# Kernel tuning notes

Measured on AMD Instinct MI355X. Metric: run time of the kernel, lower is better.

Reference implementation:

```python
import math
import jax, jax.numpy as jnp
import numpy as np

B, S, E = 4, 2048, 1024

def setup_inputs() -> dict:
    key = jax.random.key(0)
    k1, k2, k3 = jax.random.split(key, 3)
    X = jax.random.normal(k1, (B, S, E), dtype=jnp.float32)
    # nn.Linear(E, 3E): weight [3E, E], bias [3E]; scale weights for sane softmax
    W = jax.random.normal(k2, (3 * E, E), dtype=jnp.float32) * (1.0 / math.sqrt(E))
    b = jax.random.normal(k3, (3 * E,), dtype=jnp.float32) * 0.01
    return {"X": X, "W": W, "b": b}

def reference(X, W, b):
    E_ = X.shape[-1]
    # fused QKV projection: X @ W^T + b -> [B, S, 3E]
    qkv = jnp.einsum('bse,fe->bsf', X, W) + b
    q, k, v = jnp.split(qkv, 3, axis=-1)
    scores = jnp.einsum('bqe,bke->bqk', q, k) / math.sqrt(E_)
    attention_weight = jax.nn.softmax(scores, axis=-1)  # [B, S, S]
    output = jnp.einsum('bqk,bke->bqe', attention_weight, v)
    return (output, attention_weight)
```

## Files before the change

kernel.cpp:

```cpp
#include <hip/hip_runtime.h>
#include <math.h>

typedef __bf16 bf16;
typedef __bf16 bf16x4 __attribute__((ext_vector_type(4)));
typedef __bf16 bf16x8 __attribute__((ext_vector_type(8)));
typedef float f32x4 __attribute__((ext_vector_type(4)));

#define MODE_QKV    0
#define MODE_SCORES 1
#define MODE_PV     2

__device__ inline void gload_lds16(const bf16* g, bf16* l) {
    __builtin_amdgcn_global_load_lds(
        (const __attribute__((address_space(1))) void*)g,
        (__attribute__((address_space(3))) void*)l, 16, 0, 0);
}

#define DSR(dst, base, imm)                                                 \
    asm volatile("ds_read_b128 %0, %1 offset:%2"                            \
        : "=v"(dst)                                                         \
        : "v"((const __attribute__((address_space(3))) bf16*)(base)),       \
          "i"(imm))

#define MF(i, j) acc[i][j] = __builtin_amdgcn_mfma_f32_16x16x32_bf16(       \
    af[i], bq[j], acc[i][j], 0, 0, 0);

template <int MODE, int NT>
__global__ __launch_bounds__(512) void mfma_nt(
    const bf16* __restrict__ A, const bf16* __restrict__ B,
    const float* __restrict__ bias, void* __restrict__ Cv,
    int lda, int ldb, int ldc,
    long sA, long sB, long sC, float alpha)
{
    A += (long)blockIdx.z * sA;
    B += (long)blockIdx.z * sB;

    __shared__ bf16 As[3 * 8192] __attribute__((aligned(16)));
    __shared__ bf16 Bs[3 * 4096] __attribute__((aligned(16)));

    const int t  = threadIdx.x;
    const int m0 = blockIdx.y * 256;
    const int n0 = blockIdx.x * 128;

    const int lane = t & 63;
    const int wave = t >> 6;
    const int wr   = (wave >> 1) * 64;
    const int wc   = (wave & 1) * 64;
    const int fr   = lane & 15;
    const int kq8  = lane >> 4;

    const bf16* gA0; const bf16* gA1; const bf16* gB0;
    {
        const int c0 = t,        r0 = c0 >> 2, h0 = ((c0 & 3) ^ ((r0 >> 1) & 3)) * 8;
        const int c1 = t + 512,  r1 = c1 >> 2, h1 = ((c1 & 3) ^ ((r1 >> 1) & 3)) * 8;
        gA0 = A + (long)(m0 + r0) * lda + h0;
        gA1 = A + (long)(m0 + r1) * lda + h1;
        gB0 = B + (long)(n0 + r0) * ldb + h0;
    }

    const int swz = kq8 ^ ((fr >> 1) & 3);
    const bf16* pA = As + (wr + fr) * 32 + swz * 8;
    const bf16* pB = Bs + (wc + fr) * 32 + swz * 8;

    f32x4 acc[4][4] = {};
    bf16x8 af[4], bq[4];
    int kofs;

#define STAGE3(SS, ko)                                                      \
    gload_lds16(gA0 + (ko), &As[(SS) * 8192 + t * 8]);                      \
    gload_lds16(gA1 + (ko), &As[(SS) * 8192 + (t + 512) * 8]);              \
    gload_lds16(gB0 + (ko), &Bs[(SS) * 4096 + t * 8]);

#define TB(CS, STG) do {                                                    \
    DSR(af[0], pA, (CS) * 16384 + 0);                                       \
    DSR(af[1], pA, (CS) * 16384 + 1024);                                    \
    DSR(bq[0], pB, (CS) * 8192 + 0);                                        \
    DSR(bq[1], pB, (CS) * 8192 + 1024);                                     \
    DSR(bq[2], pB, (CS) * 8192 + 2048);                                     \
    DSR(bq[3], pB, (CS) * 8192 + 3072);                                     \
    DSR(af[2], pA, (CS) * 16384 + 2048);                                    \
    DSR(af[3], pA, (CS) * 16384 + 3072);                                    \
    asm volatile("s_waitcnt lgkmcnt(2)" ::: "memory");                      \
    __builtin_amdgcn_sched_barrier(0);                                      \
    __builtin_amdgcn_s_setprio(1);                                          \
    MF(0,0) MF(0,1) MF(1,0) MF(1,1)                                         \
    MF(0,2) MF(0,3) MF(1,2) MF(1,3)                                         \
    __builtin_amdgcn_s_setprio(0);                                          \
    if constexpr ((STG) == 1) { STAGE3(((CS) + 2) % 3, kofs); kofs += 32; } \
    asm volatile("s_waitcnt lgkmcnt(0)" ::: "memory");                      \
    __builtin_amdgcn_sched_barrier(0);                                      \
    __builtin_amdgcn_s_setprio(1);                                          \
    MF(2,0) MF(2,1) MF(3,0) MF(3,1)                                         \
    MF(2,2) MF(2,3) MF(3,2) MF(3,3)                                         \
    __builtin_amdgcn_s_setprio(0);                                          \
    if constexpr ((STG) == 1)                                               \
        asm volatile("s_waitcnt vmcnt(3)" ::: "memory");                    \
    else if constexpr ((STG) == 0)                                          \
        asm volatile("s_waitcnt vmcnt(0)" ::: "memory");                    \
    if constexpr ((STG) != 2) __builtin_amdgcn_s_barrier();                 \
} while (0)

    STAGE3(0, 0);
    STAGE3(1, 32);
    kofs = 64;
    asm volatile("s_waitcnt vmcnt(3)" ::: "memory");
    __builtin_amdgcn_s_barrier();

    static_assert(NT % 3 != 0, "peel pattern assumes NT%3 in {1,2}");
    if constexpr (NT % 3 == 2) {
        TB(0, 1); TB(1, 1);
        for (int g = 0; g < (NT - 5) / 3; ++g) { TB(2, 1); TB(0, 1); TB(1, 1); }
        TB(2, 1); TB(0, 0); TB(1, 2);
    } else {
        TB(0, 1);
        for (int g = 0; g < (NT - 4) / 3; ++g) { TB(1, 1); TB(2, 1); TB(0, 1); }
        TB(1, 1); TB(2, 0); TB(0, 2);
    }
#undef TB
#undef STAGE3

    const int r4 = (lane >> 4) * 4;
    if constexpr (MODE == MODE_PV) {
        float* C = (float*)Cv + (long)blockIdx.z * sC;
#pragma unroll
        for (int j = 0; j < 4; j++) {
            const int col = n0 + wc + j * 16 + fr;
#pragma unroll
            for (int i = 0; i < 4; i++)
#pragma unroll
                for (int r = 0; r < 4; r++) {
                    const long row = m0 + wr + i * 16 + r4 + r;
                    C[row * ldc + col] = acc[i][j][r];
                }
        }
    } else {
        bf16* C = (bf16*)Cv + (long)blockIdx.z * sC;
#pragma unroll
        for (int j = 0; j < 4; j++) {
            const int col = n0 + wc + j * 16 + fr;
            const float bv = (MODE == MODE_QKV) ? bias[col] : 0.f;
#pragma unroll
            for (int i = 0; i < 4; i++)
#pragma unroll
                for (int r = 0; r < 4; r++) {
                    const long row = m0 + wr + i * 16 + r4 + r;
                    float v = acc[i][j][r];
                    if constexpr (MODE == MODE_QKV)
                        C[row * ldc + col] = (bf16)(v + bv);
                    else
                        C[row * ldc + col] = (bf16)__expf(alpha * v);
                }
        }
    }
}

__global__ __launch_bounds__(256) void f32_to_bf16(
    const float* __restrict__ in, bf16* __restrict__ out, long n)
{
    long i = ((long)blockIdx.x * 256 + threadIdx.x) * 4;
    if (i < n) {
        float4 v = *(const float4*)(in + i);
        bf16x4 o = { (bf16)v.x, (bf16)v.y, (bf16)v.z, (bf16)v.w };
        *(bf16x4*)(out + i) = o;
    }
}

__global__ __launch_bounds__(256) void transpose_v(
    const bf16* __restrict__ V, bf16* __restrict__ Vt)
{
    __shared__ bf16 tile[32][33];
    const bf16* Vb  = V  + (long)blockIdx.z * 2048 * 3072;
    bf16*       Vtb = Vt + (long)blockIdx.z * 1024 * 2048;
    const int s0 = blockIdx.x * 32, e0 = blockIdx.y * 32;
    const int tx = threadIdx.x & 31, ty = threadIdx.x >> 5;
#pragma unroll
    for (int i = 0; i < 32; i += 8)
        tile[ty + i][tx] = Vb[(long)(s0 + ty + i) * 3072 + e0 + tx];
    __syncthreads();
#pragma unroll
    for (int i = 0; i < 32; i += 8)
        Vtb[(long)(e0 + ty + i) * 2048 + s0 + tx] = tile[tx][ty + i];
}

__global__ __launch_bounds__(256) void norm_rows(
    bf16* __restrict__ Pu, float* __restrict__ out1)
{
    bf16* p  = Pu   + (long)blockIdx.x * 2048;
    float* o = out1 + (long)blockIdx.x * 2048;
    const int t = threadIdx.x;
    bf16x8 v = *(const bf16x8*)(p + t * 8);
    float f[8];
    float s = 0.f;
#pragma unroll
    for (int k = 0; k < 8; k++) { f[k] = (float)v[k]; s += f[k]; }
#pragma unroll
    for (int off = 32; off > 0; off >>= 1) s += __shfl_xor(s, off);
    __shared__ float red[4];
    const int wid = t >> 6, lane = t & 63;
    if (lane == 0) red[wid] = s;
    __syncthreads();
    s = red[0] + red[1] + red[2] + red[3];
    const float inv = 1.0f / s;
    float4 a, b;
    a.x = f[0] * inv; a.y = f[1] * inv; a.z = f[2] * inv; a.w = f[3] * inv;
    b.x = f[4] * inv; b.y = f[5] * inv; b.z = f[6] * inv; b.w = f[7] * inv;
    *(float4*)(o + t * 8)     = a;
    *(float4*)(o + t * 8 + 4) = b;
    bf16x8 w;
#pragma unroll
    for (int k = 0; k < 8; k++) w[k] = (bf16)(f[k] * inv);
    *(bf16x8*)(p + t * 8) = w;
}

extern "C" void kernel_launch(void* const* d_in, const int* in_sizes, int n_in,
                              void* d_out, int out_size, void* d_ws, size_t ws_size,
                              hipStream_t stream)
{
    const int B = 4, S = 2048, E = 1024;
    const float* X    = (const float*)d_in[0];
    const float* W    = (const float*)d_in[1];
    const float* bias = (const float*)d_in[2];

    float* out0 = (float*)d_out;
    float* out1 = out0 + (long)B * S * E;

    char* ws = (char*)d_ws;
    bf16* qkvb = (bf16*)(ws);
    bf16* Vt   = (bf16*)(ws + 50331648);
    bf16* Pu   = (bf16*)(ws + 67108864);
    bf16* Xb   = (bf16*)(ws + 67108864);
    bf16* Wb   = (bf16*)(ws + 83886080);

    f32_to_bf16<<<(long)B * S * E / 1024, 256, 0, stream>>>(X, Xb, (long)B * S * E);
    f32_to_bf16<<<(long)3 * E * E / 1024, 256, 0, stream>>>(W, Wb, (long)3 * E * E);

    mfma_nt<MODE_QKV, 32><<<dim3(3 * E / 128, B * S / 256, 1), 512, 0, stream>>>(
        Xb, Wb, bias, qkvb, E, E, 3 * E, 0, 0, 0, 1.0f);

    transpose_v<<<dim3(S / 32, E / 32, B), 256, 0, stream>>>(qkvb + 2 * E, Vt);

    mfma_nt<MODE_SCORES, 32><<<dim3(S / 128, S / 256, B), 512, 0, stream>>>(
        qkvb, qkvb + E, nullptr, Pu, 3 * E, 3 * E, S,
        (long)S * 3 * E, (long)S * 3 * E, (long)S * S, 0.03125f);

    norm_rows<<<B * S, 256, 0, stream>>>(Pu, out1);

    mfma_nt<MODE_PV, 64><<<dim3(E / 128, S / 256, B), 512, 0, stream>>>(
        Pu, Vt, nullptr, out0, S, S, E,
        (long)S * S, (long)E * S, (long)S * E, 1.0f);
}
```

Baseline: 296.7 us.

## Add 256x256-tile GEMM kernel with 4-stage ring for QKV and scores

Adds a new mfma_nt256 kernel that computes 256x256 output tiles, with each wave owning 128x64. It uses a 4-deep LDS ring buffer and split A/B staging interleaved with two MFMA half-phases. The QKV projection and score GEMMs now launch this kernel with half as many blocks along N, which raises arithmetic intensity per LDS byte. The cost is double the accumulator registers (128 floats per thread), 128KB of LDS, extra barriers, and fewer blocks for occupancy and load balance.

```diff
diff --git a/kernel.cpp b/kernel.cpp
--- a/kernel.cpp
+++ b/kernel.cpp
@@ -24,6 +24,133 @@
 
 #define MF(i, j) acc[i][j] = __builtin_amdgcn_mfma_f32_16x16x32_bf16(       \
     af[i], bq[j], acc[i][j], 0, 0, 0);
+
+template <int MODE, int NT>
+__global__ __launch_bounds__(512) void mfma_nt256(
+    const bf16* __restrict__ A, const bf16* __restrict__ B,
+    const float* __restrict__ bias, void* __restrict__ Cv,
+    int lda, int ldb, int ldc,
+    long sA, long sB, long sC, float alpha)
+{
+    A += (long)blockIdx.z * sA;
+    B += (long)blockIdx.z * sB;
+
+    __shared__ bf16 As[4 * 8192] __attribute__((aligned(16)));
+    __shared__ bf16 Bs[4 * 8192] __attribute__((aligned(16)));
+
+    const int t  = threadIdx.x;
+    const int m0 = blockIdx.y * 256;
+    const int n0 = blockIdx.x * 256;
+
+    const int lane = t & 63;
+    const int wave = t >> 6;
+    const int wr   = (wave >> 2) * 128;
+    const int wc   = (wave & 3) * 64;
+    const int fr   = lane & 15;
+    const int kq8  = lane >> 4;
+
+    const bf16* gA0; const bf16* gA1; const bf16* gB0; const bf16* gB1;
+    {
+        const int c0 = t,        r0 = c0 >> 2, h0 = ((c0 & 3) ^ ((r0 >> 1) & 3)) * 8;
+        const int c1 = t + 512,  r1 = c1 >> 2, h1 = ((c1 & 3) ^ ((r1 >> 1) & 3)) * 8;
+        gA0 = A + (long)(m0 + r0) * lda + h0;
+        gA1 = A + (long)(m0 + r1) * lda + h1;
+        gB0 = B + (long)(n0 + r0) * ldb + h0;
+        gB1 = B + (long)(n0 + r1) * ldb + h1;
+    }
+
+    const int swz = kq8 ^ ((fr >> 1) & 3);
+    const bf16* pA = As + (wr + fr) * 32 + swz * 8;
+    const bf16* pB = Bs + (wc + fr) * 32 + swz * 8;
+
+    f32x4 acc[8][4] = {};
+    bf16x8 af[8], bq[4];
+    int kofs;
+
+#define STA256(SS, ko)                                                      \
+    gload_lds16(gA0 + (ko), &As[(SS) * 8192 + t * 8]);                      \
+    gload_lds16(gA1 + (ko), &As[(SS) * 8192 + (t + 512) * 8]);
+#define STB256(SS, ko)                                                      \
+    gload_lds16(gB0 + (ko), &Bs[(SS) * 8192 + t * 8]);                      \
+    gload_lds16(gB1 + (ko), &Bs[(SS) * 8192 + (t + 512) * 8]);
+
+#define TB256(S, STG) do {                                                  \
+               \
+    DSR(af[0], pA, (S) * 16384 + 0);                                        \
+    DSR(af[1], pA, (S) * 16384 + 1024);                                     \
+    DSR(af[2], pA, (S) * 16384 + 2048);                                     \
+    DSR(af[3], pA, (S) * 16384 + 3072);                                     \
+    DSR(bq[0], pB, (S) * 16384 + 0);                                        \
+    DSR(bq[1], pB, (S) * 16384 + 1024);                                     \
+    DSR(bq[2], pB, (S) * 16384 + 2048);                                     \
+    DSR(bq[3], pB, (S) * 16384 + 3072);                                     \
+    if constexpr ((STG) == 1) { STA256(((S) + 3) & 3, kofs); }              \
+    __builtin_amdgcn_s_barrier();                                           \
+    asm volatile("s_waitcnt lgkmcnt(0)" ::: "memory");                      \
+    __builtin_amdgcn_sched_barrier(0);                                      \
+    __builtin_amdgcn_s_setprio(1);                                          \
+    MF(0,0) MF(0,1) MF(0,2) MF(0,3) MF(1,0) MF(1,1) MF(1,2) MF(1,3)         \
+    MF(2,0) MF(2,1) MF(2,2) MF(2,3) MF(3,0) MF(3,1) MF(3,2) MF(3,3)         \
+    __builtin_amdgcn_s_setprio(0);                                          \
+    __builtin_amdgcn_s_barrier();                                           \
+                       \
+    DSR(af[4], pA, (S) * 16384 + 4096);                                     \
+    DSR(af[5], pA, (S) * 16384 + 5120);                                     \
+    DSR(af[6], pA, (S) * 16384 + 6144);                                     \
+    DSR(af[7], pA, (S) * 16384 + 7168);                                     \
+    if constexpr ((STG) == 1) { STB256(((S) + 3) & 3, kofs); kofs += 32; }  \
+    __builtin_amdgcn_s_barrier();                                           \
+    asm volatile("s_waitcnt lgkmcnt(0)" ::: "memory");                      \
+    __builtin_amdgcn_sched_barrier(0);                                      \
+    __builtin_amdgcn_s_setprio(1);                                          \
+    MF(4,0) MF(4,1) MF(4,2) MF(4,3) MF(5,0) MF(5,1) MF(5,2) MF(5,3)         \
+    MF(6,0) MF(6,1) MF(6,2) MF(6,3) MF(7,0) MF(7,1) MF(7,2) MF(7,3)         \
+    __builtin_amdgcn_s_setprio(0);                                          \
+    if constexpr ((STG) == 1)                                               \
+        asm volatile("s_waitcnt vmcnt(8)" ::: "memory");                    \
+    else if constexpr ((STG) == 3)                                          \
+        asm volatile("s_waitcnt vmcnt(4)" ::: "memory");                    \
+    else if constexpr ((STG) == 0)                                          \
+        asm volatile("s_waitcnt vmcnt(0)" ::: "memory");                    \
+    if constexpr ((STG) != 2) __builtin_amdgcn_s_barrier();                 \
+} while (0)
+
+    STA256(0, 0);  STB256(0, 0);
+    STA256(1, 32); STB256(1, 32);
+    STA256(2, 64); STB256(2, 64);
+    kofs = 96;
+    asm volatile("s_waitcnt vmcnt(8)" ::: "memory");
+    __builtin_amdgcn_s_barrier();
+
+    static_assert(NT % 4 == 0 && NT >= 8, "ring-4 peel assumes NT%4==0");
+    for (int g = 0; g < NT / 4 - 1; ++g) {
+        TB256(0, 1); TB256(1, 1); TB256(2, 1); TB256(3, 1);
+    }
+    TB256(0, 1);
+    TB256(1, 3); TB256(2, 0); TB256(3, 2);
+#undef TB256
+#undef STA256
+#undef STB256
+
+    const int r4 = (lane >> 4) * 4;
+    bf16* C = (bf16*)Cv + (long)blockIdx.z * sC;
+#pragma unroll
+    for (int j = 0; j < 4; j++) {
+        const int col = n0 + wc + j * 16 + fr;
+        const float bv = (MODE == MODE_QKV) ? bias[col] : 0.f;
+#pragma unroll
+        for (int i = 0; i < 8; i++)
+#pragma unroll
+            for (int r = 0; r < 4; r++) {
+                const long row = m0 + wr + i * 16 + r4 + r;
+                float v = acc[i][j][r];
+                if constexpr (MODE == MODE_QKV)
+                    C[row * ldc + col] = (bf16)(v + bv);
+                else
+                    C[row * ldc + col] = (bf16)__expf(alpha * v);
+            }
+    }
+}
 
 template <int MODE, int NT>
 __global__ __launch_bounds__(512) void mfma_nt(
@@ -70,6 +197,9 @@
     gload_lds16(gA0 + (ko), &As[(SS) * 8192 + t * 8]);                      \
     gload_lds16(gA1 + (ko), &As[(SS) * 8192 + (t + 512) * 8]);              \
     gload_lds16(gB0 + (ko), &Bs[(SS) * 4096 + t * 8]);
+
+#define MF4(i, j) acc[i][j] = __builtin_amdgcn_mfma_f32_16x16x32_bf16(      \
+    af[i], bq[j], acc[i][j], 0, 0, 0);
 
 #define TB(CS, STG) do {                                                    \
     DSR(af[0], pA, (CS) * 16384 + 0);                                       \
@@ -83,15 +213,15 @@
     asm volatile("s_waitcnt lgkmcnt(2)" ::: "memory");                      \
     __builtin_amdgcn_sched_barrier(0);                                      \
     __builtin_amdgcn_s_setprio(1);                                          \
-    MF(0,0) MF(0,1) MF(1,0) MF(1,1)                                         \
-    MF(0,2) MF(0,3) MF(1,2) MF(1,3)                                         \
+    MF4(0,0) MF4(0,1) MF4(1,0) MF4(1,1)                                     \
+    MF4(0,2) MF4(0,3) MF4(1,2) MF4(1,3)                                     \
     __builtin_amdgcn_s_setprio(0);                                          \
     if constexpr ((STG) == 1) { STAGE3(((CS) + 2) % 3, kofs); kofs += 32; } \
     asm volatile("s_waitcnt lgkmcnt(0)" ::: "memory");                      \
     __builtin_amdgcn_sched_barrier(0);                                      \
     __builtin_amdgcn_s_setprio(1);                                          \
-    MF(2,0) MF(2,1) MF(3,0) MF(3,1)                                         \
-    MF(2,2) MF(2,3) MF(3,2) MF(3,3)                                         \
+    MF4(2,0) MF4(2,1) MF4(3,0) MF4(3,1)                                     \
+    MF4(2,2) MF4(2,3) MF4(3,2) MF4(3,3)                                     \
     __builtin_amdgcn_s_setprio(0);                                          \
     if constexpr ((STG) == 1)                                               \
         asm volatile("s_waitcnt vmcnt(3)" ::: "memory");                    \
@@ -118,6 +248,7 @@
     }
 #undef TB
 #undef STAGE3
+#undef MF4
 
     const int r4 = (lane >> 4) * 4;
     if constexpr (MODE == MODE_PV) {
@@ -234,12 +365,12 @@
     f32_to_bf16<<<(long)B * S * E / 1024, 256, 0, stream>>>(X, Xb, (long)B * S * E);
     f32_to_bf16<<<(long)3 * E * E / 1024, 256, 0, stream>>>(W, Wb, (long)3 * E * E);
 
-    mfma_nt<MODE_QKV, 32><<<dim3(3 * E / 128, B * S / 256, 1), 512, 0, stream>>>(
+    mfma_nt256<MODE_QKV, 32><<<dim3(3 * E / 256, B * S / 256, 1), 512, 0, stream>>>(
         Xb, Wb, bias, qkvb, E, E, 3 * E, 0, 0, 0, 1.0f);
 
     transpose_v<<<dim3(S / 32, E / 32, B), 256, 0, stream>>>(qkvb + 2 * E, Vt);
 
-    mfma_nt<MODE_SCORES, 32><<<dim3(S / 128, S / 256, B), 512, 0, stream>>>(
+    mfma_nt256<MODE_SCORES, 32><<<dim3(S / 256, S / 256, B), 512, 0, stream>>>(
         qkvb, qkvb + E, nullptr, Pu, 3 * E, 3 * E, S,
         (long)S * 3 * E, (long)S * 3 * E, (long)S * S, 0.03125f);
 
```

Measured after the change: 317.3 us. 6.9% more time.

## Fuse V transpose into QKV epilogue and defer softmax normalization to PV

Applied to the files above, without the earlier changes.

The QKV GEMM epilogue now writes the V columns directly in transposed layout, which removes the separate transpose kernel and the padded 3E qkv buffer. The row normalization kernel no longer rewrites the bf16 probability matrix. It stores per-row inverse sums, and the PV GEMM applies them in its epilogue. The two fp32-to-bf16 conversions are merged into one launch. In exchange the transposed V stores are strided (bf16x4 per lane across rows), and PV now multiplies unnormalized bf16 exponentials, which changes rounding slightly.

```diff
diff --git a/kernel.cpp b/kernel.cpp
--- a/kernel.cpp
+++ b/kernel.cpp
@@ -29,6 +29,7 @@
 __global__ __launch_bounds__(512) void mfma_nt(
     const bf16* __restrict__ A, const bf16* __restrict__ B,
     const float* __restrict__ bias, void* __restrict__ Cv,
+    bf16* __restrict__ Vtp,
     int lda, int ldb, int ldc,
     long sA, long sB, long sC, float alpha)
 {
@@ -122,6 +123,13 @@
     const int r4 = (lane >> 4) * 4;
     if constexpr (MODE == MODE_PV) {
         float* C = (float*)Cv + (long)blockIdx.z * sC;
+        const float* Rs = bias + (long)blockIdx.z * 2048;
+        float iv[4][4];
+#pragma unroll
+        for (int i = 0; i < 4; i++)
+#pragma unroll
+            for (int r = 0; r < 4; r++)
+                iv[i][r] = Rs[m0 + wr + i * 16 + r4 + r];
 #pragma unroll
         for (int j = 0; j < 4; j++) {
             const int col = n0 + wc + j * 16 + fr;
@@ -130,62 +138,77 @@
 #pragma unroll
                 for (int r = 0; r < 4; r++) {
                     const long row = m0 + wr + i * 16 + r4 + r;
-                    C[row * ldc + col] = acc[i][j][r];
+                    C[row * ldc + col] = acc[i][j][r] * iv[i][r];
                 }
+        }
+    } else if constexpr (MODE == MODE_QKV) {
+        if (n0 >= 2048) {
+            const int  bi = m0 >> 11;
+            bf16* Vb = Vtp + (long)bi * (1024 * 2048);
+#pragma unroll
+            for (int j = 0; j < 4; j++) {
+                const int col = n0 + wc + j * 16 + fr;
+                const int e   = col - 2048;
+                const float bv = bias[col];
+#pragma unroll
+                for (int i = 0; i < 4; i++) {
+                    const int sb = (m0 + wr + i * 16 + r4) & 2047;
+                    bf16x4 o = { (bf16)(acc[i][j][0] + bv),
+                                 (bf16)(acc[i][j][1] + bv),
+                                 (bf16)(acc[i][j][2] + bv),
+                                 (bf16)(acc[i][j][3] + bv) };
+                    *(bf16x4*)&Vb[(long)e * 2048 + sb] = o;
+                }
+            }
+        } else {
+            bf16* C = (bf16*)Cv;
+#pragma unroll
+            for (int j = 0; j < 4; j++) {
+                const int col = n0 + wc + j * 16 + fr;
+                const float bv = bias[col];
+#pragma unroll
+                for (int i = 0; i < 4; i++)
+#pragma unroll
+                    for (int r = 0; r < 4; r++) {
+                        const long row = m0 + wr + i * 16 + r4 + r;
+                        C[row * ldc + col] = (bf16)(acc[i][j][r] + bv);
+                    }
+            }
         }
     } else {
         bf16* C = (bf16*)Cv + (long)blockIdx.z * sC;
 #pragma unroll
         for (int j = 0; j < 4; j++) {
             const int col = n0 + wc + j * 16 + fr;
-            const float bv = (MODE == MODE_QKV) ? bias[col] : 0.f;
 #pragma unroll
             for (int i = 0; i < 4; i++)
 #pragma unroll
                 for (int r = 0; r < 4; r++) {
                     const long row = m0 + wr + i * 16 + r4 + r;
-                    float v = acc[i][j][r];
-                    if constexpr (MODE == MODE_QKV)
-                        C[row * ldc + col] = (bf16)(v + bv);
-                    else
-                        C[row * ldc + col] = (bf16)__expf(alpha * v);
+                    C[row * ldc + col] = (bf16)__expf(alpha * acc[i][j][r]);
                 }
         }
     }
 }
 
-__global__ __launch_bounds__(256) void f32_to_bf16(
-    const float* __restrict__ in, bf16* __restrict__ out, long n)
+__global__ __launch_bounds__(256) void f32_to_bf16_2(
+    const float* __restrict__ X, bf16* __restrict__ Xb, long nX,
+    const float* __restrict__ W, bf16* __restrict__ Wb, long nW)
 {
     long i = ((long)blockIdx.x * 256 + threadIdx.x) * 4;
-    if (i < n) {
-        float4 v = *(const float4*)(in + i);
-        bf16x4 o = { (bf16)v.x, (bf16)v.y, (bf16)v.z, (bf16)v.w };
-        *(bf16x4*)(out + i) = o;
-    }
-}
-
-__global__ __launch_bounds__(256) void transpose_v(
-    const bf16* __restrict__ V, bf16* __restrict__ Vt)
-{
-    __shared__ bf16 tile[32][33];
-    const bf16* Vb  = V  + (long)blockIdx.z * 2048 * 3072;
-    bf16*       Vtb = Vt + (long)blockIdx.z * 1024 * 2048;
-    const int s0 = blockIdx.x * 32, e0 = blockIdx.y * 32;
-    const int tx = threadIdx.x & 31, ty = threadIdx.x >> 5;
-#pragma unroll
-    for (int i = 0; i < 32; i += 8)
-        tile[ty + i][tx] = Vb[(long)(s0 + ty + i) * 3072 + e0 + tx];
-    __syncthreads();
-#pragma unroll
-    for (int i = 0; i < 32; i += 8)
-        Vtb[(long)(e0 + ty + i) * 2048 + s0 + tx] = tile[tx][ty + i];
+    const float* in; bf16* out; long idx;
+    if (i < nX) { in = X; out = Xb; idx = i; }
+    else        { in = W; out = Wb; idx = i - nX; if (idx >= nW) return; }
+    float4 v = *(const float4*)(in + idx);
+    bf16x4 o = { (bf16)v.x, (bf16)v.y, (bf16)v.z, (bf16)v.w };
+    *(bf16x4*)(out + idx) = o;
 }
 
 __global__ __launch_bounds__(256) void norm_rows(
-    bf16* __restrict__ Pu, float* __restrict__ out1)
-{
-    bf16* p  = Pu   + (long)blockIdx.x * 2048;
+    const bf16* __restrict__ Pu, float* __restrict__ out1,
+    float* __restrict__ rs)
+{
+    const bf16* p = Pu  + (long)blockIdx.x * 2048;
     float* o = out1 + (long)blockIdx.x * 2048;
     const int t = threadIdx.x;
     bf16x8 v = *(const bf16x8*)(p + t * 8);
@@ -201,15 +224,12 @@
     __syncthreads();
     s = red[0] + red[1] + red[2] + red[3];
     const float inv = 1.0f / s;
+    if (t == 0) rs[blockIdx.x] = inv;
     float4 a, b;
     a.x = f[0] * inv; a.y = f[1] * inv; a.z = f[2] * inv; a.w = f[3] * inv;
     b.x = f[4] * inv; b.y = f[5] * inv; b.z = f[6] * inv; b.w = f[7] * inv;
     *(float4*)(o + t * 8)     = a;
     *(float4*)(o + t * 8 + 4) = b;
-    bf16x8 w;
-#pragma unroll
-    for (int k = 0; k < 8; k++) w[k] = (bf16)(f[k] * inv);
-    *(bf16x8*)(p + t * 8) = w;
 }
 
 extern "C" void kernel_launch(void* const* d_in, const int* in_sizes, int n_in,
@@ -225,27 +245,27 @@
     float* out1 = out0 + (long)B * S * E;
 
     char* ws = (char*)d_ws;
-    bf16* qkvb = (bf16*)(ws);
-    bf16* Vt   = (bf16*)(ws + 50331648);
-    bf16* Pu   = (bf16*)(ws + 67108864);
-    bf16* Xb   = (bf16*)(ws + 67108864);
-    bf16* Wb   = (bf16*)(ws + 83886080);
-
-    f32_to_bf16<<<(long)B * S * E / 1024, 256, 0, stream>>>(X, Xb, (long)B * S * E);
-    f32_to_bf16<<<(long)3 * E * E / 1024, 256, 0, stream>>>(W, Wb, (long)3 * E * E);
+    bf16*  qkvb = (bf16*)(ws);
+    bf16*  Vt   = (bf16*)(ws + 33554432);
+    float* rs   = (float*)(ws + 50331648);
+    bf16*  Pu   = (bf16*)(ws + 67108864);
+    bf16*  Xb   = (bf16*)(ws + 67108864);
+    bf16*  Wb   = (bf16*)(ws + 83886080);
+
+    const long nX = (long)B * S * E;
+    const long nW = (long)3 * E * E;
+    f32_to_bf16_2<<<(nX + nW) / 1024, 256, 0, stream>>>(X, Xb, nX, W, Wb, nW);
 
     mfma_nt<MODE_QKV, 32><<<dim3(3 * E / 128, B * S / 256, 1), 512, 0, stream>>>(
-        Xb, Wb, bias, qkvb, E, E, 3 * E, 0, 0, 0, 1.0f);
-
-    transpose_v<<<dim3(S / 32, E / 32, B), 256, 0, stream>>>(qkvb + 2 * E, Vt);
+        Xb, Wb, bias, qkvb, Vt, E, E, 2048, 0, 0, 0, 1.0f);
 
     mfma_nt<MODE_SCORES, 32><<<dim3(S / 128, S / 256, B), 512, 0, stream>>>(
-        qkvb, qkvb + E, nullptr, Pu, 3 * E, 3 * E, S,
-        (long)S * 3 * E, (long)S * 3 * E, (long)S * S, 0.03125f);
-
-    norm_rows<<<B * S, 256, 0, stream>>>(Pu, out1);
+        qkvb, qkvb + 1024, nullptr, Pu, nullptr, 2048, 2048, S,
+        (long)S * 2048, (long)S * 2048, (long)S * S, 0.03125f);
+
+    norm_rows<<<B * S, 256, 0, stream>>>(Pu, out1, rs);
 
     mfma_nt<MODE_PV, 64><<<dim3(E / 128, S / 256, B), 512, 0, stream>>>(
-        Pu, Vt, nullptr, out0, S, S, E,
+        Pu, Vt, rs, out0, nullptr, S, S, E,
         (long)S * S, (long)E * S, (long)S * E, 1.0f);
 }
```

Measured after the change: 288.9 us (median of 2 runs). -2.6%, faster.
